# Optimization experiments

Hardware: AMD Instinct MI355X
Metric: run time of the kernel (lower is better)

Reference implementation:

```python
import jax, jax.numpy as jnp
import numpy as np

B, N, H, I = 64, 1000, 128, 64  # batch, nodes, hidden_dim, loc-embed intermediate
BN_EPS = 1e-5
NEG_SLOPE = 0.2


def setup_inputs() -> dict:
    key = jax.random.key(0)
    ks = jax.random.split(key, 24)
    s = lambda k, shape, sc=0.05: (jax.random.normal(k, shape) * sc).astype(jnp.float32)
    d = {}
    d["locs"] = jax.random.uniform(ks[0], (B, N, 2), dtype=jnp.float32)
    # LocationEmbedding params (num_layers=1 hidden block)
    d["le_W0"] = s(ks[1], (2, I));   d["le_b0"] = jnp.zeros((I,), jnp.float32)
    d["le_W1"] = s(ks[2], (I, I));   d["le_b1"] = jnp.zeros((I,), jnp.float32)
    d["le_bn_g"] = 1.0 + s(ks[3], (I,), 0.1)
    d["le_bn_b"] = s(ks[4], (I,), 0.1)
    d["le_bn_m"] = s(ks[5], (I,), 0.1)
    d["le_bn_v"] = 0.5 + jax.random.uniform(ks[6], (I,), dtype=jnp.float32)
    d["le_Wo"] = s(ks[7], (I, H));   d["le_bo"] = jnp.zeros((H,), jnp.float32)
    # 3 GATConv layers (heads=1): lin weight (no bias), att_src, att_dst, output bias
    d["gat_W"] = s(ks[8], (3, H, H))
    d["gat_asrc"] = s(ks[9], (3, H))
    d["gat_adst"] = s(ks[10], (3, H))
    d["gat_b"] = jnp.zeros((3, H), jnp.float32)
    # 2 BatchNorm layers between GAT layers (eval mode: running stats)
    d["bn_g"] = 1.0 + s(ks[11], (2, H), 0.1)
    d["bn_b"] = s(ks[12], (2, H), 0.1)
    d["bn_m"] = s(ks[13], (2, H), 0.1)
    d["bn_v"] = 0.5 + jax.random.uniform(ks[14], (2, H), dtype=jnp.float32)
    return d


def _bn(x, g, b, m, v):
    return (x - m) * jax.lax.rsqrt(v + BN_EPS) * g + b


def _gat(x, W, a_src, a_dst, bias):
    # Dense fully-connected GAT (heads=1, self-loops included).
    h = jnp.einsum('bnc,cd->bnd', x, W)          # [B,N,H]
    e_src = jnp.einsum('bnd,d->bn', h, a_src)    # alpha contribution of source j
    e_dst = jnp.einsum('bnd,d->bn', h, a_dst)    # alpha contribution of target i
    e = e_src[:, None, :] + e_dst[:, :, None]    # e[b,i,j] for edge j->i
    e = jnp.where(e > 0, e, NEG_SLOPE * e)       # leaky_relu(0.2)
    alpha = jax.nn.softmax(e, axis=-1)           # softmax over sources j per target i
    return jnp.einsum('bij,bjc->bic', alpha, h) + bias


def reference(locs, le_W0, le_b0, le_W1, le_b1, le_bn_g, le_bn_b, le_bn_m, le_bn_v,
              le_Wo, le_bo, gat_W, gat_asrc, gat_adst, gat_b, bn_g, bn_b, bn_m, bn_v):
    # LocationEmbedding: Linear -> ReLU -> [Linear -> BN -> ReLU -> (dropout: eval)] -> Linear
    z = jax.nn.relu(locs @ le_W0 + le_b0)
    z = jax.nn.relu(_bn(z @ le_W1 + le_b1, le_bn_g, le_bn_b, le_bn_m, le_bn_v))
    x = z @ le_Wo + le_bo                        # [B,N,H]
    # [GAT -> BN -> ReLU -> (dropout: eval)] x2 -> GAT
    for l in range(2):
        x = _gat(x, gat_W[l], gat_asrc[l], gat_adst[l], gat_b[l])
        x = jax.nn.relu(_bn(x, bn_g[l], bn_b[l], bn_m[l], bn_v[l]))
    x = _gat(x, gat_W[2], gat_asrc[2], gat_adst[2], gat_b[2])
    return x                                     # [B,N,H]
```

## Files before the change

kernel.cpp:

```cpp
#include <hip/hip_runtime.h>
#include <hip/hip_bf16.h>

#define BN_EPS 1e-5f
#define NB 64
#define NN 1000
#define NP 1024
#define HD 128
#define CS 8
#define NC 125

typedef short bf16x8 __attribute__((ext_vector_type(8)));
typedef float f32x4 __attribute__((ext_vector_type(4)));

__device__ __forceinline__ unsigned short f2b(float f) {
  __hip_bfloat16 h = __float2bfloat16(f);
  return *reinterpret_cast<unsigned short*>(&h);
}
__device__ __forceinline__ float b2f(unsigned short u) {
  unsigned v = ((unsigned)u) << 16;
  return __uint_as_float(v);
}
__device__ __forceinline__ unsigned tkey(float f) {
  unsigned u = __float_as_uint(f);
  return u ^ ((unsigned)((int)u >> 31) | 0x80000000u);
}
__device__ __forceinline__ float tdec(unsigned m) {
  unsigned u = (m & 0x80000000u) ? (m ^ 0x80000000u) : ~m;
  return __uint_as_float(u);
}

__global__ __launch_bounds__(256) void k_embed(
    const float* __restrict__ locs,
    const float* __restrict__ W0, const float* __restrict__ b0,
    const float* __restrict__ W1, const float* __restrict__ b1,
    const float* __restrict__ g1, const float* __restrict__ be1,
    const float* __restrict__ m1, const float* __restrict__ v1,
    const float* __restrict__ Wo, const float* __restrict__ bo,
    const float* __restrict__ gatW, unsigned short* __restrict__ WT,
    unsigned short* __restrict__ xb) {
  __shared__ float z1T[64][68];
  __shared__ float z2T[64][68];
  int tid = threadIdx.x;
  long base = (long)blockIdx.x * 64;

  if (blockIdx.x < 192) {
    int idx = blockIdx.x * 256 + tid;
    int lay = idx >> 14, rem = idx & 16383;
    int n = rem >> 7, kk = rem & 127;
    WT[idx] = f2b(gatW[lay * 16384 + kk * 128 + n]);
  }

  {
    int d = tid & 63;
    int q = tid >> 6;
    float w0x = W0[d], w0y = W0[64 + d], bb = b0[d];
#pragma unroll
    for (int g = 0; g < 4; ++g) {
      float vv[4];
#pragma unroll
      for (int i = 0; i < 4; ++i) {
        int n = g * 16 + q * 4 + i;
        float lx = locs[(base + n) * 2 + 0];
        float ly = locs[(base + n) * 2 + 1];
        vv[i] = fmaxf(fmaf(lx, w0x, fmaf(ly, w0y, bb)), 0.f);
      }
      *(float4*)&z1T[d][g * 16 + q * 4] = make_float4(vv[0], vv[1], vv[2], vv[3]);
    }
  }
  __syncthreads();

  int nt = tid & 15;
  int dt = tid >> 4;

  {
    float acc[4][4];
#pragma unroll
    for (int i = 0; i < 4; ++i)
#pragma unroll
      for (int j = 0; j < 4; ++j) acc[i][j] = 0.f;
#pragma unroll 4
    for (int k = 0; k < 64; ++k) {
      float4 zv = *(const float4*)&z1T[k][4 * nt];
      float4 wv = *(const float4*)&W1[k * 64 + 4 * dt];
      float zz[4] = {zv.x, zv.y, zv.z, zv.w};
      float ww[4] = {wv.x, wv.y, wv.z, wv.w};
#pragma unroll
      for (int i = 0; i < 4; ++i)
#pragma unroll
        for (int j = 0; j < 4; ++j) acc[i][j] = fmaf(zz[i], ww[j], acc[i][j]);
    }
    float4 b1v = *(const float4*)&b1[4 * dt];
    float4 g1v = *(const float4*)&g1[4 * dt];
    float4 bev = *(const float4*)&be1[4 * dt];
    float4 m1v = *(const float4*)&m1[4 * dt];
    float4 v1v = *(const float4*)&v1[4 * dt];
    float bbv[4] = {b1v.x, b1v.y, b1v.z, b1v.w};
    float ggv[4] = {g1v.x, g1v.y, g1v.z, g1v.w};
    float eev[4] = {bev.x, bev.y, bev.z, bev.w};
    float mmv[4] = {m1v.x, m1v.y, m1v.z, m1v.w};
    float vvv[4] = {v1v.x, v1v.y, v1v.z, v1v.w};
#pragma unroll
    for (int j = 0; j < 4; ++j) {
      float sc = ggv[j] * rsqrtf(vvv[j] + BN_EPS);
      float sh = eev[j] - mmv[j] * sc;
      float o[4];
#pragma unroll
      for (int i = 0; i < 4; ++i)
        o[i] = fmaxf(fmaf(acc[i][j] + bbv[j], sc, sh), 0.f);
      *(float4*)&z2T[4 * dt + j][4 * nt] = make_float4(o[0], o[1], o[2], o[3]);
    }
  }
  __syncthreads();

  {
    float acc[4][8];
#pragma unroll
    for (int i = 0; i < 4; ++i)
#pragma unroll
      for (int j = 0; j < 8; ++j) acc[i][j] = 0.f;
#pragma unroll 2
    for (int k = 0; k < 64; ++k) {
      float4 zv = *(const float4*)&z2T[k][4 * nt];
      float4 wa = *(const float4*)&Wo[k * 128 + 4 * dt];
      float4 wb = *(const float4*)&Wo[k * 128 + 64 + 4 * dt];
      float zz[4] = {zv.x, zv.y, zv.z, zv.w};
      float w0[4] = {wa.x, wa.y, wa.z, wa.w};
      float w1[4] = {wb.x, wb.y, wb.z, wb.w};
#pragma unroll
      for (int i = 0; i < 4; ++i) {
#pragma unroll
        for (int j = 0; j < 4; ++j) {
          acc[i][j] = fmaf(zz[i], w0[j], acc[i][j]);
          acc[i][4 + j] = fmaf(zz[i], w1[j], acc[i][4 + j]);
        }
      }
    }
    float4 bo0 = *(const float4*)&bo[4 * dt];
    float4 bo1 = *(const float4*)&bo[64 + 4 * dt];
    float bb0[4] = {bo0.x, bo0.y, bo0.z, bo0.w};
    float bb1[4] = {bo1.x, bo1.y, bo1.z, bo1.w};
#pragma unroll
    for (int i = 0; i < 4; ++i) {
      ushort4 p0, p1;
      p0.x = f2b(acc[i][0] + bb0[0]); p0.y = f2b(acc[i][1] + bb0[1]);
      p0.z = f2b(acc[i][2] + bb0[2]); p0.w = f2b(acc[i][3] + bb0[3]);
      p1.x = f2b(acc[i][4] + bb1[0]); p1.y = f2b(acc[i][5] + bb1[1]);
      p1.z = f2b(acc[i][6] + bb1[2]); p1.w = f2b(acc[i][7] + bb1[3]);
      *(ushort4*)&xb[(base + 4 * nt + i) * 128 + 4 * dt] = p0;
      *(ushort4*)&xb[(base + 4 * nt + i) * 128 + 64 + 4 * dt] = p1;
    }
  }
}

__global__ __launch_bounds__(256) void k_gemm_e(
    const unsigned short* __restrict__ xb, const unsigned short* __restrict__ WT,
    const float* __restrict__ asrc, const float* __restrict__ adst,
    unsigned short* __restrict__ hb, float* __restrict__ es,
    float* __restrict__ ed) {
  int tid = threadIdx.x;
  int w = tid >> 6, l = tid & 63;
  long rowbase = (long)blockIdx.x * 64 + w * 16;
  int r = l & 15, g = l >> 4;

  f32x4 acc[8];
#pragma unroll
  for (int n = 0; n < 8; ++n) acc[n] = {0.f, 0.f, 0.f, 0.f};

#pragma unroll
  for (int ks = 0; ks < 4; ++ks) {
    bf16x8 a = *(const bf16x8*)&xb[(rowbase + r) * 128 + ks * 32 + g * 8];
#pragma unroll
    for (int n = 0; n < 8; ++n) {
      bf16x8 bfr = *(const bf16x8*)&WT[(n * 16 + r) * 128 + ks * 32 + g * 8];
      acc[n] = __builtin_amdgcn_mfma_f32_16x16x32_bf16(a, bfr, acc[n], 0, 0, 0);
    }
  }

  float ps[4] = {0.f, 0.f, 0.f, 0.f};
  float pd[4] = {0.f, 0.f, 0.f, 0.f};
#pragma unroll
  for (int n = 0; n < 8; ++n) {
    float sa = asrc[n * 16 + r];
    float sd = adst[n * 16 + r];
#pragma unroll
    for (int rr = 0; rr < 4; ++rr) {
      float v = acc[n][rr];
      hb[(rowbase + g * 4 + rr) * 128 + n * 16 + r] = f2b(v);
      ps[rr] = fmaf(v, sa, ps[rr]);
      pd[rr] = fmaf(v, sd, pd[rr]);
    }
  }
#pragma unroll
  for (int rr = 0; rr < 4; ++rr) {
#pragma unroll
    for (int m = 1; m <= 8; m <<= 1) {
      ps[rr] += __shfl_xor(ps[rr], m, 64);
      pd[rr] += __shfl_xor(pd[rr], m, 64);
    }
  }
  if (r == 0) {
#pragma unroll
    for (int rr = 0; rr < 4; ++rr) {
      es[rowbase + g * 4 + rr] = ps[rr];
      ed[rowbase + g * 4 + rr] = pd[rr];
    }
  }
}

#define CEX(a, b, up)                         \
  do {                                        \
    if (((a) > (b)) == (up)) {                \
      unsigned long long _t = (a);            \
      (a) = (b);                              \
      (b) = _t;                               \
    }                                         \
  } while (0)

__global__ __launch_bounds__(512) void k_scpfx(
    const float* __restrict__ es, const float* __restrict__ ed,
    const unsigned short* __restrict__ hb, float2* __restrict__ e12,
    int* __restrict__ kcut, float2* __restrict__ ab, float* __restrict__ C1,
    float* __restrict__ C2, unsigned short* __restrict__ hs) {
  __shared__ unsigned long long keys[NP];
  __shared__ float smem[(NC + 1) * 64];
  __shared__ float2 wtot[8];
  float2* sc = (float2*)smem;
  float (*s1)[32] = (float(*)[32])smem;
  float (*s2)[32] = (float(*)[32])(smem + (NC + 1) * 32);
  int tid = threadIdx.x, b = blockIdx.x, dq = blockIdx.y;

  for (int i = tid; i < NP; i += 512) {
    unsigned long long kk;
    if (i < NN) {
      kk = ((unsigned long long)tkey(es[b * NN + i]) << 32) | (unsigned)i;
    } else {
      kk = (0xFF800000ull << 32) | (unsigned)i;
    }
    keys[i] = kk;
  }
  __syncthreads();
  int i0 = tid * 2;
  {
    unsigned long long q0 = keys[i0], q1 = keys[i0 + 1];
    CEX(q0, q1, (i0 & 2) == 0);
    keys[i0] = q0; keys[i0 + 1] = q1;
  }
  __syncthreads();
  for (int k = 4; k <= NP; k <<= 1) {
    for (int j = k >> 1; j >= 2; j >>= 1) {
      int i = ((tid & ~(j - 1)) << 1) | (tid & (j - 1));
      int ixj = i | j;
      bool up = ((i & k) == 0);
      unsigned long long a = keys[i], c = keys[ixj];
      if ((a > c) == up) { keys[i] = c; keys[ixj] = a; }
      __syncthreads();
    }
    {
      unsigned long long q0 = keys[i0], q1 = keys[i0 + 1];
      CEX(q0, q1, (i0 & k) == 0);
      keys[i0] = q0; keys[i0 + 1] = q1;
    }
    __syncthreads();
  }

  float2 f0 = make_float2(0.f, 0.f), f1 = make_float2(0.f, 0.f);
  {
    unsigned long long k0 = keys[i0], k1 = keys[i0 + 1];
    if (i0 < NN) {
      float s = tdec((unsigned)(k0 >> 32));
      f0.x = __expf(s);
      f0.y = __expf(0.2f * s);
      if (dq == 0) e12[b * NN + i0] = f0;
    }
    if (i0 + 1 < NN) {
      float s = tdec((unsigned)(k1 >> 32));
      f1.x = __expf(s);
      f1.y = __expf(0.2f * s);
      if (dq == 0) e12[b * NN + i0 + 1] = f1;
    }
  }
  int lane = tid & 63, wid = tid >> 6;
  float tx = f0.x + f1.x, ty = f0.y + f1.y;
  float ix = tx, iy = ty;
#pragma unroll
  for (int dlt = 1; dlt < 64; dlt <<= 1) {
    float ox = __shfl_up(ix, dlt, 64);
    float oy = __shfl_up(iy, dlt, 64);
    if (lane >= dlt) { ix += ox; iy += oy; }
  }
  if (lane == 63) wtot[wid] = make_float2(ix, iy);
  __syncthreads();
  float bx = 0.f, by = 0.f;
#pragma unroll
  for (int ww = 0; ww < 8; ++ww) {
    if (ww < wid) {
      float2 t = wtot[ww];
      bx += t.x;
      by += t.y;
    }
  }
  float exx = bx + ix - tx, eyy = by + iy - ty;
  float in0x = exx + f0.x, in0y = eyy + f0.y;
  if (i0 < NN) sc[i0] = make_float2(in0x, in0y);
  if (i0 + 1 < NN) sc[i0 + 1] = make_float2(in0x + f1.x, in0y + f1.y);
  __syncthreads();

  if (dq == 0) {
    float s1tot = sc[NN - 1].x;
    for (int i = tid; i < NN; i += 512) {
      float di = ed[b * NN + i];
      unsigned tt = tkey(-di);
      int lo = 0, hi = NP;
      while (lo < hi) {
        int mid = (lo + hi) >> 1;
        if ((unsigned)(keys[mid] >> 32) <= tt) lo = mid + 1; else hi = mid;
      }
      int k = lo;
      float p1 = (k > 0) ? sc[k - 1].x : 0.f;
      float p2 = (k > 0) ? sc[k - 1].y : 0.f;
      float Ed = __expf(di);
      float Ed2 = __expf(0.2f * di);
      float den = fmaf(Ed, s1tot - p1, Ed2 * p2);
      kcut[b * NN + i] = k;
      ab[b * NN + i] = make_float2(Ed / den, Ed2 / den);
    }
  }
  __syncthreads();

  int d = tid & 31;
  int cl = tid >> 5;
  int dglob = dq * 32 + d;
  for (int c = cl; c < NC; c += 16) {
    float v1 = 0.f, v2 = 0.f;
#pragma unroll
    for (int u = 0; u < CS; ++u) {
      int j = c * CS + u;
      unsigned long long kk = keys[j];
      int p = (int)(unsigned)kk;
      float s = tdec((unsigned)(kk >> 32));
      float e1 = __expf(s), e2 = __expf(0.2f * s);
      unsigned short hraw = hb[((long)b * NN + p) * HD + dglob];
      hs[((long)b * NN + j) * HD + dglob] = hraw;
      float hv = b2f(hraw);
      v1 = fmaf(e1, hv, v1);
      v2 = fmaf(e2, hv, v2);
    }
    s1[c][d] = v1;
    s2[c][d] = v2;
  }
  __syncthreads();

  if (tid < 32) {
    float r = 0.f;
    for (int c = 0; c < NC; ++c) {
      float v = s1[c][tid];
      s1[c][tid] = r;
      r += v;
    }
    s1[NC][tid] = r;
  } else if (tid < 64) {
    int dd = tid - 32;
    float r = 0.f;
    for (int c = 0; c < NC; ++c) {
      float v = s2[c][dd];
      s2[c][dd] = r;
      r += v;
    }
    s2[NC][dd] = r;
  }
  __syncthreads();

  long basec = (long)b * (NC + 1) * HD + dq * 32;
  for (int i = tid; i < (NC + 1) * 32; i += 512) {
    int c = i >> 5, dd = i & 31;
    C1[basec + (long)c * HD + dd] = s1[c][dd];
    C2[basec + (long)c * HD + dd] = s2[c][dd];
  }
}

template <bool APPLY_BN>
__global__ __launch_bounds__(128) void k_out(
    const unsigned short* __restrict__ hs, const float* __restrict__ C1,
    const float* __restrict__ C2, const float2* __restrict__ e12,
    const int* __restrict__ kcut, const float2* __restrict__ ab,
    const float* __restrict__ bias, const float* __restrict__ bng,
    const float* __restrict__ bnb, const float* __restrict__ bnm,
    const float* __restrict__ bnv, float* __restrict__ xo,
    unsigned short* __restrict__ xbo) {
  int d = threadIdx.x, b = blockIdx.x;
  int i0 = blockIdx.y * 8;
  float T1 = C1[((long)b * (NC + 1) + NC) * HD + d];
  float bs = bias[d];
  float sc = 0.f, sh = 0.f;
  if (APPLY_BN) {
    float g = bng[d], bb = bnb[d], m = bnm[d], v = bnv[d];
    sc = g * rsqrtf(v + BN_EPS);
    sh = bb - m * sc;
  }
  for (int i = i0; i < i0 + 8; ++i) {
    int k = kcut[b * NN + i];
    float2 coeff = ab[b * NN + i];
    int c = k >> 3;
    float base1 = C1[((long)b * (NC + 1) + c) * HD + d];
    float base2 = C2[((long)b * (NC + 1) + c) * HD + d];
    float p1 = 0.f, p2 = 0.f;
    for (int j = c * CS; j < k; ++j) {
      float hv = b2f(hs[((long)b * NN + j) * HD + d]);
      float2 e = e12[b * NN + j];
      p1 = fmaf(e.x, hv, p1);
      p2 = fmaf(e.y, hv, p2);
    }
    float val = fmaf(coeff.x, T1 - base1 - p1, fmaf(coeff.y, base2 + p2, bs));
    long off = ((long)b * NN + i) * HD + d;
    if (APPLY_BN) {
      xbo[off] = f2b(fmaxf(fmaf(val, sc, sh), 0.f));
    } else {
      xo[off] = val;
    }
  }
}

extern "C" void kernel_launch(void* const* d_in, const int* in_sizes, int n_in,
                              void* d_out, int out_size, void* d_ws,
                              size_t ws_size, hipStream_t stream) {
  const float* locs = (const float*)d_in[0];
  const float* le_W0 = (const float*)d_in[1];
  const float* le_b0 = (const float*)d_in[2];
  const float* le_W1 = (const float*)d_in[3];
  const float* le_b1 = (const float*)d_in[4];
  const float* le_bn_g = (const float*)d_in[5];
  const float* le_bn_b = (const float*)d_in[6];
  const float* le_bn_m = (const float*)d_in[7];
  const float* le_bn_v = (const float*)d_in[8];
  const float* le_Wo = (const float*)d_in[9];
  const float* le_bo = (const float*)d_in[10];
  const float* gat_W = (const float*)d_in[11];
  const float* gat_asrc = (const float*)d_in[12];
  const float* gat_adst = (const float*)d_in[13];
  const float* gat_b = (const float*)d_in[14];
  const float* bn_g = (const float*)d_in[15];
  const float* bn_b = (const float*)d_in[16];
  const float* bn_m = (const float*)d_in[17];
  const float* bn_v = (const float*)d_in[18];

  float* out = (float*)d_out;
  unsigned short* hb = (unsigned short*)d_ws;
  unsigned short* hs = hb + 8192000;
  unsigned short* xb = hs + 8192000;
  unsigned short* WT = xb + 8192000;
  float* C1 = (float*)(WT + 49152 + 64);
  float* C2 = C1 + 1032192;
  float* es = C2 + 1032192;
  float* ed = es + 64000;
  float2* e12 = (float2*)(ed + 64000);
  float2* ab = e12 + 64000;
  int* kcut = (int*)(ab + 64000);

  k_embed<<<1000, 256, 0, stream>>>(locs, le_W0, le_b0, le_W1, le_b1, le_bn_g,
                                    le_bn_b, le_bn_m, le_bn_v, le_Wo, le_bo,
                                    gat_W, WT, xb);
  for (int l = 0; l < 3; ++l) {
    k_gemm_e<<<1000, 256, 0, stream>>>(xb, WT + l * 16384,
                                       gat_asrc + l * 128, gat_adst + l * 128,
                                       hb, es, ed);
    k_scpfx<<<dim3(NB, 4), 512, 0, stream>>>(es, ed, hb, e12, kcut, ab, C1,
                                             C2, hs);
    if (l < 2) {
      k_out<true><<<dim3(NB, NC), 128, 0, stream>>>(
          hs, C1, C2, e12, kcut, ab, gat_b + l * 128, bn_g + l * 128,
          bn_b + l * 128, bn_m + l * 128, bn_v + l * 128, nullptr, xb);
    } else {
      k_out<false><<<dim3(NB, NC), 128, 0, stream>>>(
          hs, C1, C2, e12, kcut, ab, gat_b + 2 * 128, nullptr, nullptr,
          nullptr, nullptr, out, nullptr);
    }
  }
}
```

Baseline: 209.8 us.

## Fuse embedding with first GAT projection and interleave prefix-sum buffers

Weight transposition moves into its own small kernel. The location embedding now keeps its bf16 output in shared memory and runs the layer-0 MFMA projection and attention-score reductions in the same kernel, which avoids writing xb to global memory and reading it back. The C1 and C2 prefix arrays are merged into one interleaved float2 buffer, so k_out does a single wider load per access. The cost is one extra kernel launch for weight prep and higher shared memory and register use in the fused kernel.

```diff
diff --git a/kernel.cpp b/kernel.cpp
--- a/kernel.cpp
+++ b/kernel.cpp
@@ -8,6 +8,7 @@
 #define HD 128
 #define CS 8
 #define NC 125
+#define XS 136
 
 typedef short bf16x8 __attribute__((ext_vector_type(8)));
 typedef float f32x4 __attribute__((ext_vector_type(4)));
@@ -29,26 +30,30 @@
   return __uint_as_float(u);
 }
 
-__global__ __launch_bounds__(256) void k_embed(
+__global__ __launch_bounds__(256) void k_wprep(const float* __restrict__ W,
+                                               unsigned short* __restrict__ WT) {
+  int idx = blockIdx.x * 256 + threadIdx.x;
+  int lay = idx >> 14, rem = idx & 16383;
+  int n = rem >> 7, k = rem & 127;
+  WT[idx] = f2b(W[lay * 16384 + k * 128 + n]);
+}
+
+__global__ __launch_bounds__(256) void k_embed_gemm(
     const float* __restrict__ locs,
     const float* __restrict__ W0, const float* __restrict__ b0,
     const float* __restrict__ W1, const float* __restrict__ b1,
     const float* __restrict__ g1, const float* __restrict__ be1,
     const float* __restrict__ m1, const float* __restrict__ v1,
     const float* __restrict__ Wo, const float* __restrict__ bo,
-    const float* __restrict__ gatW, unsigned short* __restrict__ WT,
-    unsigned short* __restrict__ xb) {
+    const unsigned short* __restrict__ WT,
+    const float* __restrict__ asrc, const float* __restrict__ adst,
+    unsigned short* __restrict__ hb, float* __restrict__ es,
+    float* __restrict__ ed) {
   __shared__ float z1T[64][68];
   __shared__ float z2T[64][68];
+  unsigned short* xs = (unsigned short*)&z1T[0][0];
   int tid = threadIdx.x;
   long base = (long)blockIdx.x * 64;
-
-  if (blockIdx.x < 192) {
-    int idx = blockIdx.x * 256 + tid;
-    int lay = idx >> 14, rem = idx & 16383;
-    int n = rem >> 7, kk = rem & 127;
-    WT[idx] = f2b(gatW[lay * 16384 + kk * 128 + n]);
-  }
 
   {
     int d = tid & 63;
@@ -146,8 +151,56 @@
       p0.z = f2b(acc[i][2] + bb0[2]); p0.w = f2b(acc[i][3] + bb0[3]);
       p1.x = f2b(acc[i][4] + bb1[0]); p1.y = f2b(acc[i][5] + bb1[1]);
       p1.z = f2b(acc[i][6] + bb1[2]); p1.w = f2b(acc[i][7] + bb1[3]);
-      *(ushort4*)&xb[(base + 4 * nt + i) * 128 + 4 * dt] = p0;
-      *(ushort4*)&xb[(base + 4 * nt + i) * 128 + 64 + 4 * dt] = p1;
+      *(ushort4*)&xs[(4 * nt + i) * XS + 4 * dt] = p0;
+      *(ushort4*)&xs[(4 * nt + i) * XS + 64 + 4 * dt] = p1;
+    }
+  }
+  __syncthreads();
+
+  {
+    int w = tid >> 6, l = tid & 63;
+    long rowbase = base + w * 16;
+    int r = l & 15, g = l >> 4;
+    f32x4 acc[8];
+#pragma unroll
+    for (int n = 0; n < 8; ++n) acc[n] = {0.f, 0.f, 0.f, 0.f};
+#pragma unroll
+    for (int ks = 0; ks < 4; ++ks) {
+      bf16x8 a = *(const bf16x8*)&xs[(w * 16 + r) * XS + ks * 32 + g * 8];
+#pragma unroll
+      for (int n = 0; n < 8; ++n) {
+        bf16x8 bfr = *(const bf16x8*)&WT[(n * 16 + r) * 128 + ks * 32 + g * 8];
+        acc[n] = __builtin_amdgcn_mfma_f32_16x16x32_bf16(a, bfr, acc[n], 0, 0, 0);
+      }
+    }
+    float ps[4] = {0.f, 0.f, 0.f, 0.f};
+    float pd[4] = {0.f, 0.f, 0.f, 0.f};
+#pragma unroll
+    for (int n = 0; n < 8; ++n) {
+      float sa = asrc[n * 16 + r];
+      float sd = adst[n * 16 + r];
+#pragma unroll
+      for (int rr = 0; rr < 4; ++rr) {
+        float v = acc[n][rr];
+        hb[(rowbase + g * 4 + rr) * 128 + n * 16 + r] = f2b(v);
+        ps[rr] = fmaf(v, sa, ps[rr]);
+        pd[rr] = fmaf(v, sd, pd[rr]);
+      }
+    }
+#pragma unroll
+    for (int rr = 0; rr < 4; ++rr) {
+#pragma unroll
+      for (int m = 1; m <= 8; m <<= 1) {
+        ps[rr] += __shfl_xor(ps[rr], m, 64);
+        pd[rr] += __shfl_xor(pd[rr], m, 64);
+      }
+    }
+    if (r == 0) {
+#pragma unroll
+      for (int rr = 0; rr < 4; ++rr) {
+        es[rowbase + g * 4 + rr] = ps[rr];
+        ed[rowbase + g * 4 + rr] = pd[rr];
+      }
     }
   }
 }
@@ -219,8 +272,8 @@
 __global__ __launch_bounds__(512) void k_scpfx(
     const float* __restrict__ es, const float* __restrict__ ed,
     const unsigned short* __restrict__ hb, float2* __restrict__ e12,
-    int* __restrict__ kcut, float2* __restrict__ ab, float* __restrict__ C1,
-    float* __restrict__ C2, unsigned short* __restrict__ hs) {
+    int* __restrict__ kcut, float2* __restrict__ ab, float2* __restrict__ C12,
+    unsigned short* __restrict__ hs) {
   __shared__ unsigned long long keys[NP];
   __shared__ float smem[(NC + 1) * 64];
   __shared__ float2 wtot[8];
@@ -373,23 +426,21 @@
   long basec = (long)b * (NC + 1) * HD + dq * 32;
   for (int i = tid; i < (NC + 1) * 32; i += 512) {
     int c = i >> 5, dd = i & 31;
-    C1[basec + (long)c * HD + dd] = s1[c][dd];
-    C2[basec + (long)c * HD + dd] = s2[c][dd];
+    C12[basec + (long)c * HD + dd] = make_float2(s1[c][dd], s2[c][dd]);
   }
 }
 
 template <bool APPLY_BN>
 __global__ __launch_bounds__(128) void k_out(
-    const unsigned short* __restrict__ hs, const float* __restrict__ C1,
-    const float* __restrict__ C2, const float2* __restrict__ e12,
-    const int* __restrict__ kcut, const float2* __restrict__ ab,
-    const float* __restrict__ bias, const float* __restrict__ bng,
-    const float* __restrict__ bnb, const float* __restrict__ bnm,
-    const float* __restrict__ bnv, float* __restrict__ xo,
-    unsigned short* __restrict__ xbo) {
+    const unsigned short* __restrict__ hs, const float2* __restrict__ C12,
+    const float2* __restrict__ e12, const int* __restrict__ kcut,
+    const float2* __restrict__ ab, const float* __restrict__ bias,
+    const float* __restrict__ bng, const float* __restrict__ bnb,
+    const float* __restrict__ bnm, const float* __restrict__ bnv,
+    float* __restrict__ xo, unsigned short* __restrict__ xbo) {
   int d = threadIdx.x, b = blockIdx.x;
   int i0 = blockIdx.y * 8;
-  float T1 = C1[((long)b * (NC + 1) + NC) * HD + d];
+  float T1 = C12[((long)b * (NC + 1) + NC) * HD + d].x;
   float bs = bias[d];
   float sc = 0.f, sh = 0.f;
   if (APPLY_BN) {
@@ -401,8 +452,7 @@
     int k = kcut[b * NN + i];
     float2 coeff = ab[b * NN + i];
     int c = k >> 3;
-    float base1 = C1[((long)b * (NC + 1) + c) * HD + d];
-    float base2 = C2[((long)b * (NC + 1) + c) * HD + d];
+    float2 base12 = C12[((long)b * (NC + 1) + c) * HD + d];
     float p1 = 0.f, p2 = 0.f;
     for (int j = c * CS; j < k; ++j) {
       float hv = b2f(hs[((long)b * NN + j) * HD + d]);
@@ -410,7 +460,8 @@
       p1 = fmaf(e.x, hv, p1);
       p2 = fmaf(e.y, hv, p2);
     }
-    float val = fmaf(coeff.x, T1 - base1 - p1, fmaf(coeff.y, base2 + p2, bs));
+    float val = fmaf(coeff.x, T1 - base12.x - p1,
+                     fmaf(coeff.y, base12.y + p2, bs));
     long off = ((long)b * NN + i) * HD + d;
     if (APPLY_BN) {
       xbo[off] = f2b(fmaxf(fmaf(val, sc, sh), 0.f));
@@ -448,31 +499,34 @@
   unsigned short* hs = hb + 8192000;
   unsigned short* xb = hs + 8192000;
   unsigned short* WT = xb + 8192000;
-  float* C1 = (float*)(WT + 49152 + 64);
-  float* C2 = C1 + 1032192;
-  float* es = C2 + 1032192;
+  float2* C12 = (float2*)(WT + 49152 + 64);
+  float* es = (float*)(C12 + 1032192);
   float* ed = es + 64000;
   float2* e12 = (float2*)(ed + 64000);
   float2* ab = e12 + 64000;
   int* kcut = (int*)(ab + 64000);
 
-  k_embed<<<1000, 256, 0, stream>>>(locs, le_W0, le_b0, le_W1, le_b1, le_bn_g,
-                                    le_bn_b, le_bn_m, le_bn_v, le_Wo, le_bo,
-                                    gat_W, WT, xb);
+  k_wprep<<<192, 256, 0, stream>>>(gat_W, WT);
   for (int l = 0; l < 3; ++l) {
-    k_gemm_e<<<1000, 256, 0, stream>>>(xb, WT + l * 16384,
-                                       gat_asrc + l * 128, gat_adst + l * 128,
-                                       hb, es, ed);
-    k_scpfx<<<dim3(NB, 4), 512, 0, stream>>>(es, ed, hb, e12, kcut, ab, C1,
-                                             C2, hs);
+    if (l == 0) {
+      k_embed_gemm<<<1000, 256, 0, stream>>>(
+          locs, le_W0, le_b0, le_W1, le_b1, le_bn_g, le_bn_b, le_bn_m,
+          le_bn_v, le_Wo, le_bo, WT, gat_asrc, gat_adst, hb, es, ed);
+    } else {
+      k_gemm_e<<<1000, 256, 0, stream>>>(xb, WT + l * 16384,
+                                         gat_asrc + l * 128,
+                                         gat_adst + l * 128, hb, es, ed);
+    }
+    k_scpfx<<<dim3(NB, 4), 512, 0, stream>>>(es, ed, hb, e12, kcut, ab, C12,
+                                             hs);
     if (l < 2) {
       k_out<true><<<dim3(NB, NC), 128, 0, stream>>>(
-          hs, C1, C2, e12, kcut, ab, gat_b + l * 128, bn_g + l * 128,
+          hs, C12, e12, kcut, ab, gat_b + l * 128, bn_g + l * 128,
           bn_b + l * 128, bn_m + l * 128, bn_v + l * 128, nullptr, xb);
     } else {
       k_out<false><<<dim3(NB, NC), 128, 0, stream>>>(
-          hs, C1, C2, e12, kcut, ab, gat_b + 2 * 128, nullptr, nullptr,
-          nullptr, nullptr, out, nullptr);
-    }
-  }
-}
+          hs, C12, e12, kcut, ab, gat_b + 2 * 128, nullptr, nullptr, nullptr,
+          nullptr, out, nullptr);
+    }
+  }
+}
```

New measurement: 206.8 us. Within noise of the previous version (-1.4%).
